# Performance work log

Measured on AMD Instinct MI355X. Metric: run time of the kernel, lower is better.

The kernel has to match this reference:

```python
import jax, jax.numpy as jnp
import numpy as np


def setup_inputs() -> dict:
    key = jax.random.key(0)
    k1, k2, k3, k4 = jax.random.split(key, 4)
    B, OPT, IN, OUT = 16384, 64, 128, 128
    stddev = 1.0 / np.sqrt(IN)
    inputs = jax.random.normal(k1, (B, IN), dtype=jnp.float32)
    # haiku TruncatedNormal(stddev) init approximated with truncated normal
    w = jax.random.truncated_normal(k2, -2.0, 2.0, (OPT, IN, OUT), dtype=jnp.float32) * stddev
    b = jnp.zeros((OPT, OUT), dtype=jnp.float32)  # init=zeros; use random for a nontrivial check
    b = jax.random.normal(k3, (OPT, OUT), dtype=jnp.float32) * 0.02
    indices = jax.random.randint(k4, (B,), 0, OPT, dtype=jnp.int64)
    return {"inputs": inputs, "w": w, "b": b, "indices": indices}


def reference(inputs, w, b, indices):
    # out[i] = inputs[i] @ w[indices[i]] + b[indices[i]]
    # Faithful to vmap(jnp.dot)(inputs, w[indices]): gather per-example weight
    # matrices then batched matvec.
    wg = w[indices]                              # [B, IN, OUT] gathered weights
    out = jnp.einsum('bi,bio->bo', inputs, wg)   # [B, OUT]
    return out + b[indices]
```

## Files before the change

### kernel.cpp

```cpp
#include <hip/hip_runtime.h>


#define B_TOT     16384
#define NOPT      64
#define DIN       128
#define DOUT      128
#define NSLICE    16
#define SLICE_LEN (B_TOT / NSLICE)
#define NTHREADS  256
#define SP        136

typedef __attribute__((ext_vector_type(8))) short  short8;
typedef __attribute__((ext_vector_type(4))) float  floatx4;

static __device__ __forceinline__ short f2bf(float f) {
    union { float f; unsigned u; } v; v.f = f;
    unsigned r = v.u + 0x7fffu + ((v.u >> 16) & 1u);
    return (short)(r >> 16);
}

__global__ __launch_bounds__(NTHREADS)
void convert_wT_kernel(const float* __restrict__ w, unsigned short* __restrict__ wT) {
    const int o = blockIdx.x & 63;
    const int p = blockIdx.x >> 6;
    const int t = threadIdx.x;
    const int nn = p * 32 + (t & 31);
    const float* wo = w + (size_t)o * DIN * DOUT;
    unsigned short* wto = wT + (size_t)o * DIN * DOUT;
    #pragma unroll
    for (int it = 0; it < 2; ++it) {
        const int c = (t >> 5) + 8 * it;
        short8 v;
        #pragma unroll
        for (int j = 0; j < 8; ++j)
            v[j] = f2bf(wo[(size_t)(c * 8 + j) * DOUT + nn]);
        *(short8*)(wto + (size_t)nn * DIN + c * 8) = v;
    }
}

__global__ __launch_bounds__(NTHREADS)
void multilinear_kernel(const float* __restrict__ x,
                        const unsigned short* __restrict__ wT,
                        const float* __restrict__ bias,
                        const int*   __restrict__ idx,
                        float* __restrict__ out) {
    __shared__ int s_list[SLICE_LEN];
    __shared__ int s_cnt;
    __shared__ unsigned short s_w[DOUT * SP];

    const int bid = blockIdx.x;
    const int o   = bid & 63;
    const int s   = bid >> 6;
    const int t   = threadIdx.x;

    if (t == 0) s_cnt = 0;
    __syncthreads();

    const int base = s * SLICE_LEN;
    #pragma unroll
    for (int k = 0; k < SLICE_LEN / NTHREADS; ++k) {
        int i = base + t + k * NTHREADS;
        if (idx[i] == o) {
            int p = atomicAdd(&s_cnt, 1);
            s_list[p] = i;
        }
    }

    const unsigned short* wto = wT + (size_t)o * DIN * DOUT;
    #pragma unroll
    for (int it = 0; it < 8; ++it) {
        const int e16 = it * NTHREADS + t;
        const int n   = e16 >> 4;
        const int c   = e16 & 15;
        short8 v = *(const short8*)(wto + (size_t)n * DIN + c * 8);
        *(short8*)(&s_w[n * SP + c * 8]) = v;
    }
    __syncthreads();

    const int count = s_cnt;
    if (count == 0) return;

    const int wave = t >> 6;
    const int lane = t & 63;
    const int l15  = lane & 15;
    const int quad = lane >> 4;

    const int n0 = (wave * 2 + 0) * 16 + l15;
    const int n1 = (wave * 2 + 1) * 16 + l15;
    const float bv0 = bias[o * DOUT + n0];
    const float bv1 = bias[o * DOUT + n1];

    const int mtiles = (count + 15) >> 4;
    for (int mt = 0; mt < mtiles; ++mt) {
        int am = mt * 16 + l15;
        int arid = s_list[am < count ? am : count - 1];
        const float* xr = x + (size_t)arid * DIN;

        floatx4 acc0 = {0.f, 0.f, 0.f, 0.f};
        floatx4 acc1 = {0.f, 0.f, 0.f, 0.f};
        #pragma unroll
        for (int kb = 0; kb < 4; ++kb) {
            const int k0 = kb * 32 + quad * 8;
            float4 xa = *(const float4*)(xr + k0);
            float4 xb = *(const float4*)(xr + k0 + 4);
            short8 af;
            af[0] = f2bf(xa.x); af[1] = f2bf(xa.y);
            af[2] = f2bf(xa.z); af[3] = f2bf(xa.w);
            af[4] = f2bf(xb.x); af[5] = f2bf(xb.y);
            af[6] = f2bf(xb.z); af[7] = f2bf(xb.w);
            short8 b0 = *(const short8*)(&s_w[n0 * SP + k0]);
            short8 b1 = *(const short8*)(&s_w[n1 * SP + k0]);
            acc0 = __builtin_amdgcn_mfma_f32_16x16x32_bf16(af, b0, acc0, 0, 0, 0);
            acc1 = __builtin_amdgcn_mfma_f32_16x16x32_bf16(af, b1, acc1, 0, 0, 0);
        }

        #pragma unroll
        for (int r = 0; r < 4; ++r) {
            const int m = mt * 16 + quad * 4 + r;
            if (m < count) {
                const int rid = s_list[m];
                out[(size_t)rid * DOUT + n0] = acc0[r] + bv0;
                out[(size_t)rid * DOUT + n1] = acc1[r] + bv1;
            }
        }
    }
}

extern "C" void kernel_launch(void* const* d_in, const int* in_sizes, int n_in,
                              void* d_out, int out_size, void* d_ws, size_t ws_size,
                              hipStream_t stream) {
    const float* x    = (const float*)d_in[0];
    const float* w    = (const float*)d_in[1];
    const float* bias = (const float*)d_in[2];
    const int*   idx  = (const int*)d_in[3];
    float* out        = (float*)d_out;
    unsigned short* wT = (unsigned short*)d_ws;

    convert_wT_kernel<<<NOPT * 4, NTHREADS, 0, stream>>>(w, wT);
    multilinear_kernel<<<NOPT * NSLICE, NTHREADS, 0, stream>>>(x, wT, bias, idx, out);
}
```

Baseline: 76.43 us.

## Fuse weight bf16 conversion into main kernel and hold B fragments in registers

Removes the separate transpose/convert kernel. Each block now reads the fp32 weight slice for its option directly, converts it to bf16 and stores it into k-major LDS. The B fragments are then gathered once into registers, so the MFMA loop no longer reads weights from LDS. The slice count is halved to 8, so each weight matrix is loaded and converted by fewer blocks, and the row list is stored as ushort with vectorized int4 index scans. Each block still redundantly converts the full weight matrix, and the per-element strided LDS gathers may cause bank conflicts.

```diff
diff --git a/kernel.cpp b/kernel.cpp
--- a/kernel.cpp
+++ b/kernel.cpp
@@ -5,10 +5,10 @@
 #define NOPT      64
 #define DIN       128
 #define DOUT      128
-#define NSLICE    16
+#define NSLICE    8
 #define SLICE_LEN (B_TOT / NSLICE)
 #define NTHREADS  256
-#define SP        136
+#define SPN       132
 
 typedef __attribute__((ext_vector_type(8))) short  short8;
 typedef __attribute__((ext_vector_type(4))) float  floatx4;
@@ -19,61 +19,47 @@
     return (short)(r >> 16);
 }
 
-__global__ __launch_bounds__(NTHREADS)
-void convert_wT_kernel(const float* __restrict__ w, unsigned short* __restrict__ wT) {
-    const int o = blockIdx.x & 63;
-    const int p = blockIdx.x >> 6;
-    const int t = threadIdx.x;
-    const int nn = p * 32 + (t & 31);
-    const float* wo = w + (size_t)o * DIN * DOUT;
-    unsigned short* wto = wT + (size_t)o * DIN * DOUT;
-    #pragma unroll
-    for (int it = 0; it < 2; ++it) {
-        const int c = (t >> 5) + 8 * it;
-        short8 v;
-        #pragma unroll
-        for (int j = 0; j < 8; ++j)
-            v[j] = f2bf(wo[(size_t)(c * 8 + j) * DOUT + nn]);
-        *(short8*)(wto + (size_t)nn * DIN + c * 8) = v;
-    }
-}
-
-__global__ __launch_bounds__(NTHREADS)
+__global__ __launch_bounds__(NTHREADS, 4)
 void multilinear_kernel(const float* __restrict__ x,
-                        const unsigned short* __restrict__ wT,
+                        const float* __restrict__ w,
                         const float* __restrict__ bias,
                         const int*   __restrict__ idx,
                         float* __restrict__ out) {
-    __shared__ int s_list[SLICE_LEN];
+    __shared__ __align__(16) unsigned short s_w[DIN * SPN];
+    __shared__ unsigned short s_list[SLICE_LEN];
     __shared__ int s_cnt;
-    __shared__ unsigned short s_w[DOUT * SP];
 
-    const int bid = blockIdx.x;
-    const int o   = bid & 63;
-    const int s   = bid >> 6;
-    const int t   = threadIdx.x;
+    const int o = blockIdx.x & (NOPT - 1);
+    const int s = blockIdx.x >> 6;
+    const int t = threadIdx.x;
 
     if (t == 0) s_cnt = 0;
     __syncthreads();
 
-    const int base = s * SLICE_LEN;
+    const float* wo = w + (size_t)o * (DIN * DOUT);
     #pragma unroll
-    for (int k = 0; k < SLICE_LEN / NTHREADS; ++k) {
-        int i = base + t + k * NTHREADS;
-        if (idx[i] == o) {
-            int p = atomicAdd(&s_cnt, 1);
-            s_list[p] = i;
-        }
+    for (int it = 0; it < 16; ++it) {
+        const int e = it * NTHREADS + t;
+        const int k = e >> 5;
+        const int c = e & 31;
+        float4 v = ((const float4*)wo)[e];
+        ushort4 h;
+        h.x = (unsigned short)f2bf(v.x); h.y = (unsigned short)f2bf(v.y);
+        h.z = (unsigned short)f2bf(v.z); h.w = (unsigned short)f2bf(v.w);
+        *(ushort4*)(&s_w[k * SPN + c * 4]) = h;
     }
 
-    const unsigned short* wto = wT + (size_t)o * DIN * DOUT;
+    const int base = s * SLICE_LEN;
+    const int4* ip = (const int4*)(idx + base);
     #pragma unroll
-    for (int it = 0; it < 8; ++it) {
-        const int e16 = it * NTHREADS + t;
-        const int n   = e16 >> 4;
-        const int c   = e16 & 15;
-        short8 v = *(const short8*)(wto + (size_t)n * DIN + c * 8);
-        *(short8*)(&s_w[n * SP + c * 8]) = v;
+    for (int it = 0; it < SLICE_LEN / (4 * NTHREADS); ++it) {
+        const int e = it * NTHREADS + t;
+        int4 v = ip[e];
+        const int i0 = base + e * 4;
+        if (v.x == o) s_list[atomicAdd(&s_cnt, 1)] = (unsigned short)(i0 + 0);
+        if (v.y == o) s_list[atomicAdd(&s_cnt, 1)] = (unsigned short)(i0 + 1);
+        if (v.z == o) s_list[atomicAdd(&s_cnt, 1)] = (unsigned short)(i0 + 2);
+        if (v.w == o) s_list[atomicAdd(&s_cnt, 1)] = (unsigned short)(i0 + 3);
     }
     __syncthreads();
 
@@ -85,15 +71,27 @@
     const int l15  = lane & 15;
     const int quad = lane >> 4;
 
-    const int n0 = (wave * 2 + 0) * 16 + l15;
-    const int n1 = (wave * 2 + 1) * 16 + l15;
+    const int n0 = (wave * 2) * 16 + l15;
+    const int n1 = n0 + 16;
+
+    short8 bf[4][2];
+    #pragma unroll
+    for (int kb = 0; kb < 4; ++kb) {
+        #pragma unroll
+        for (int j = 0; j < 8; ++j) {
+            const int k = kb * 32 + quad * 8 + j;
+            bf[kb][0][j] = (short)s_w[k * SPN + n0];
+            bf[kb][1][j] = (short)s_w[k * SPN + n1];
+        }
+    }
+
     const float bv0 = bias[o * DOUT + n0];
     const float bv1 = bias[o * DOUT + n1];
 
     const int mtiles = (count + 15) >> 4;
     for (int mt = 0; mt < mtiles; ++mt) {
-        int am = mt * 16 + l15;
-        int arid = s_list[am < count ? am : count - 1];
+        const int am = mt * 16 + l15;
+        const int arid = s_list[am < count ? am : count - 1];
         const float* xr = x + (size_t)arid * DIN;
 
         floatx4 acc0 = {0.f, 0.f, 0.f, 0.f};
@@ -108,10 +106,8 @@
             af[2] = f2bf(xa.z); af[3] = f2bf(xa.w);
             af[4] = f2bf(xb.x); af[5] = f2bf(xb.y);
             af[6] = f2bf(xb.z); af[7] = f2bf(xb.w);
-            short8 b0 = *(const short8*)(&s_w[n0 * SP + k0]);
-            short8 b1 = *(const short8*)(&s_w[n1 * SP + k0]);
-            acc0 = __builtin_amdgcn_mfma_f32_16x16x32_bf16(af, b0, acc0, 0, 0, 0);
-            acc1 = __builtin_amdgcn_mfma_f32_16x16x32_bf16(af, b1, acc1, 0, 0, 0);
+            acc0 = __builtin_amdgcn_mfma_f32_16x16x32_bf16(af, bf[kb][0], acc0, 0, 0, 0);
+            acc1 = __builtin_amdgcn_mfma_f32_16x16x32_bf16(af, bf[kb][1], acc1, 0, 0, 0);
         }
 
         #pragma unroll
@@ -134,8 +130,6 @@
     const float* bias = (const float*)d_in[2];
     const int*   idx  = (const int*)d_in[3];
     float* out        = (float*)d_out;
-    unsigned short* wT = (unsigned short*)d_ws;
 
-    convert_wT_kernel<<<NOPT * 4, NTHREADS, 0, stream>>>(w, wT);
-    multilinear_kernel<<<NOPT * NSLICE, NTHREADS, 0, stream>>>(x, wT, bias, idx, out);
+    multilinear_kernel<<<NOPT * NSLICE, NTHREADS, 0, stream>>>(x, w, bias, idx, out);
 }
```

Result: faster. 74.73 us, median of 2 (-2.2%).
